# Optimization experiments

Measured on AMD Instinct MI355X. Metric: run time of the kernel, lower is better.

Reference implementation:

```python
import jax, jax.numpy as jnp
import numpy as np

N_QUBITS = 12
N_LAYERS = 2
IN_DIM = 16
BATCH = 4096
EPS = 1e-6
C64 = jnp.complex64


def _rz(t):
    return jnp.diag(jnp.stack([jnp.exp(-0.5j * t), jnp.exp(0.5j * t)]).astype(C64))


def _ry(t):
    c = jnp.cos(0.5 * t); s = jnp.sin(0.5 * t)
    return jnp.stack([jnp.stack([c, -s]), jnp.stack([s, c])]).astype(C64)


def _su2(p):
    # SU2: RZ(p0) then RY(p1) then RZ(p2)  ->  U = RZ(p2) @ RY(p1) @ RZ(p0)
    return _rz(p[2]) @ _ry(p[1]) @ _rz(p[0])


def _ising_xx(t):
    c = jnp.cos(0.5 * t).astype(C64); is_ = (-1j * jnp.sin(0.5 * t)).astype(C64)
    M = jnp.zeros((4, 4), C64)
    M = M.at[(0, 1, 2, 3), (0, 1, 2, 3)].set(c)
    M = M.at[(0, 1, 2, 3), (3, 2, 1, 0)].set(is_)
    return M


def _ising_yy(t):
    c = jnp.cos(0.5 * t).astype(C64); is_ = (-1j * jnp.sin(0.5 * t)).astype(C64)
    M = jnp.zeros((4, 4), C64)
    M = M.at[(0, 1, 2, 3), (0, 1, 2, 3)].set(c)
    M = M.at[(1, 2), (2, 1)].set(is_)
    M = M.at[(0, 3), (3, 0)].set(-is_)
    return M


def _ising_zz(t):
    sign = jnp.array([1.0, -1.0, -1.0, 1.0])
    return jnp.diag(jnp.exp(-0.5j * t * sign).astype(C64))


def _apply_1q(state, U, w):
    # state: [B] + [2]*n ; U: [2,2] (shared) or [B,2,2] (per-sample)
    st = jnp.moveaxis(state, w + 1, -1)
    if U.ndim == 2:
        st = jnp.einsum('...i,ji->...j', st, U)
    else:
        st = jnp.einsum('b...i,bji->b...j', st, U)
    return jnp.moveaxis(st, -1, w + 1)


def _apply_2q(state, U, w0, w1):
    st = jnp.moveaxis(state, (w0 + 1, w1 + 1), (-2, -1))
    shp = st.shape
    st = st.reshape(shp[:-2] + (4,))
    st = jnp.einsum('...i,ji->...j', st, U)
    return jnp.moveaxis(st.reshape(shp), (-2, -1), (w0 + 1, w1 + 1))


def _apply_zz_batched(state, theta, w0, w1):
    # IsingZZ is diagonal: multiply by per-sample phases, no matmul needed
    st = jnp.moveaxis(state, (w0 + 1, w1 + 1), (-2, -1))
    sign = jnp.array([[1.0, -1.0], [-1.0, 1.0]])
    ph = jnp.exp(-0.5j * theta[:, None, None] * sign).astype(C64)
    ph = ph.reshape((ph.shape[0],) + (1,) * (st.ndim - 3) + (2, 2))
    return jnp.moveaxis(st * ph, (-2, -1), (w0 + 1, w1 + 1))


def _forward(x, W, b, params):
    n = N_QUBITS
    B = x.shape[0]
    qfeat = x @ W.T + b  # NQE linear front-end -> [B, n_qubits] angles
    state = jnp.zeros((B, 2 ** n), C64).at[:, 0].set(1.0).reshape((B,) + (2,) * n)
    # --- data embedding (n_layers repetitions of RY + nearest-neighbor IsingZZ) ---
    c = jnp.cos(0.5 * qfeat); s = jnp.sin(0.5 * qfeat)
    for _ in range(N_LAYERS):
        for q in range(n):
            U = jnp.stack([jnp.stack([c[:, q], -s[:, q]], -1),
                           jnp.stack([s[:, q], c[:, q]], -1)], -2).astype(C64)  # [B,2,2]
            state = _apply_1q(state, U, q)
        for q in range(n - 1):
            state = _apply_zz_batched(state, qfeat[:, q] * qfeat[:, q + 1], q, q + 1)
    # --- SU4 brickwork ansatz (shared params across batch) ---
    g1 = n // 2; g2 = (n - 1) // 2
    layout = [(2 * i, 2 * i + 1) for i in range(g1)] + [(2 * i + 1, 2 * i + 2) for i in range(g2)]
    p = 0
    for a, bq in layout:
        pp = params[p:p + 15]; p += 15
        state = _apply_1q(state, _su2(pp[0:3]), a)
        state = _apply_1q(state, _su2(pp[3:6]), bq)
        state = _apply_2q(state, _ising_xx(pp[6]), a, bq)   # cartan_sign='ising'
        state = _apply_2q(state, _ising_yy(pp[7]), a, bq)
        state = _apply_2q(state, _ising_zz(pp[8]), a, bq)
        state = _apply_1q(state, _su2(pp[9:12]), a)
        state = _apply_1q(state, _su2(pp[12:15]), bq)
    state = _apply_1q(state, _su2(params[p:p + 3]), 0)
    # <Z_0> = P(q0=0) - P(q0=1)
    probs = jnp.sum(jnp.abs(state.reshape(B, 2, -1)) ** 2, axis=-1)
    y = (probs[:, 0] - probs[:, 1] + 1.0) * 0.5
    return jnp.clip(y, EPS, 1.0 - EPS)


def setup_inputs():
    key = jax.random.key(0)
    k1, k2, k3 = jax.random.split(key, 3)
    x = jax.random.normal(k1, (BATCH, IN_DIM), jnp.float32)
    W = jax.random.normal(k2, (N_QUBITS, IN_DIM), jnp.float32) * 0.3
    b = jnp.zeros((N_QUBITS,), jnp.float32)
    n_params = 15 * (N_QUBITS // 2 + (N_QUBITS - 1) // 2) + 3  # = 168
    params = jax.random.normal(k3, (n_params,), jnp.float32) * 0.1
    return {"x": x, "W": W, "b": b, "params": params}


def reference(x, W, b, params):
    return _forward(x, W, b, params)
```

## Files before the change

kernel.cpp:

```cpp
#include <hip/hip_runtime.h>
#include <math.h>

__device__ __forceinline__ float2 cmul(float2 a, float2 b) {
    return make_float2(a.x*b.x - a.y*b.y, a.x*b.y + a.y*b.x);
}
__device__ __forceinline__ float2 cadd(float2 a, float2 b) {
    return make_float2(a.x + b.x, a.y + b.y);
}
__device__ __forceinline__ float2 cfma2(float2 a, float2 b, float2 c) {
    c.x = fmaf(a.x, b.x, fmaf(-a.y, b.y, c.x));
    c.y = fmaf(a.x, b.y, fmaf( a.y, b.x, c.y));
    return c;
}

__device__ __forceinline__ void build_su2(const float* __restrict__ p, float2 U[2][2]) {
    float sb, cb;
    sincosf(0.5f * p[1], &sb, &cb);
    float ap = 0.5f * (p[0] + p[2]);
    float am = 0.5f * (p[0] - p[2]);
    float sap, cap, sam, cam;
    sincosf(ap, &sap, &cap);
    sincosf(am, &sam, &cam);
    U[0][0] = make_float2( cb * cap, -cb * sap);
    U[0][1] = make_float2(-sb * cam, -sb * sam);
    U[1][0] = make_float2( sb * cam, -sb * sam);
    U[1][1] = make_float2( cb * cap,  cb * sap);
}

__global__ void qcnn_setup(const float* __restrict__ params, float* __restrict__ g) {
    if (threadIdx.x != 0 || blockIdx.x != 0) return;
    const float* pp = params;
    float2 A1[2][2], B1[2][2], A2[2][2], B2[2][2];
    build_su2(pp + 0,  A1);
    build_su2(pp + 3,  B1);
    build_su2(pp + 9,  A2);
    build_su2(pp + 12, B2);
    float thx = pp[6], thy = pp[7], thz = pp[8];
    float Sa, Ca, Sb, Cb, sz, cz;
    sincosf(0.5f * (thx - thy), &Sa, &Ca);
    sincosf(0.5f * (thx + thy), &Sb, &Cb);
    sincosf(0.5f * thz, &sz, &cz);
    float2 pz  = make_float2(cz, -sz);
    float2 pzc = make_float2(cz,  sz);
    float2 K00 = make_float2(Ca * pz.x,  Ca * pz.y);
    float2 K03 = cmul(make_float2(0.f, -Sa), pz);
    float2 K11 = make_float2(Cb * pzc.x, Cb * pzc.y);
    float2 K12 = cmul(make_float2(0.f, -Sb), pzc);

    float2 T0[4][4], M1[4][4], T2[4][4];
    #pragma unroll
    for (int i = 0; i < 2; ++i)
        #pragma unroll
        for (int jj = 0; jj < 2; ++jj)
            #pragma unroll
            for (int k = 0; k < 2; ++k)
                #pragma unroll
                for (int l = 0; l < 2; ++l) {
                    T0[2*i+jj][2*k+l] = cmul(A1[i][k], B1[jj][l]);
                    T2[2*i+jj][2*k+l] = cmul(A2[i][k], B2[jj][l]);
                }
    #pragma unroll
    for (int c = 0; c < 4; ++c) {
        M1[0][c] = cadd(cmul(K00, T0[0][c]), cmul(K03, T0[3][c]));
        M1[1][c] = cadd(cmul(K11, T0[1][c]), cmul(K12, T0[2][c]));
        M1[2][c] = cadd(cmul(K12, T0[1][c]), cmul(K11, T0[2][c]));
        M1[3][c] = cadd(cmul(K03, T0[0][c]), cmul(K00, T0[3][c]));
    }
    #pragma unroll
    for (int r = 0; r < 4; ++r)
        #pragma unroll
        for (int c = 0; c < 4; ++c) {
            float2 a = make_float2(0.f, 0.f);
            #pragma unroll
            for (int k = 0; k < 4; ++k) a = cfma2(T2[r][k], M1[k][c], a);
            g[2*(4*r+c)]     = a.x;
            g[2*(4*r+c) + 1] = a.y;
        }

    float2 F[2][2];
    build_su2(params + 165, F);
    float n00 = F[0][0].x*F[0][0].x + F[0][0].y*F[0][0].y;
    float n10 = F[1][0].x*F[1][0].x + F[1][0].y*F[1][0].y;
    float n01 = F[0][1].x*F[0][1].x + F[0][1].y*F[0][1].y;
    float n11 = F[1][1].x*F[1][1].x + F[1][1].y*F[1][1].y;
    g[32] = n00 - n10;
    g[33] = n01 - n11;
    float mr = (F[0][0].x*F[0][1].x + F[0][0].y*F[0][1].y)
             - (F[1][0].x*F[1][1].x + F[1][0].y*F[1][1].y);
    float mi = (F[0][0].x*F[0][1].y - F[0][0].y*F[0][1].x)
             - (F[1][0].x*F[1][1].y - F[1][0].y*F[1][1].x);
    g[34] = mr;
    g[35] = mi;
}

__global__ __launch_bounds__(64) void qcnn_main(
    const float* __restrict__ x,
    const float* __restrict__ W,
    const float* __restrict__ bias,
    const float* __restrict__ g,
    float* __restrict__ out,
    int n)
{
    const int tid = blockIdx.x * 64 + threadIdx.x;
    if (tid >= n) return;

    float2 E[16];
    #pragma unroll
    for (int e = 0; e < 16; ++e) E[e] = make_float2(g[2*e], g[2*e+1]);
    const float m00 = g[32], m11 = g[33], mr = g[34], mi = g[35];

    const float* xr = x + tid * 16;
    float xv[16];
    #pragma unroll
    for (int k = 0; k < 16; ++k) xv[k] = xr[k];
    float qf[4];
    #pragma unroll
    for (int q = 0; q < 4; ++q) {
        const float* wr = W + q * 16;
        float acc = bias[q];
        #pragma unroll
        for (int k = 0; k < 16; ++k) acc = fmaf(xv[k], wr[k], acc);
        qf[q] = acc;
    }
    float c[4], s[4];
    #pragma unroll
    for (int q = 0; q < 4; ++q) sincosf(0.5f * qf[q], &s[q], &c[q]);
    float zs01, zc01, zs12, zc12, zs23, zc23;
    sincosf(0.5f * qf[0] * qf[1], &zs01, &zc01);
    sincosf(0.5f * qf[1] * qf[2], &zs12, &zc12);
    sincosf(0.5f * qf[2] * qf[3], &zs23, &zc23);
    const float2 f01e = make_float2(zc01, -zs01), f01d = make_float2(zc01, zs01);
    const float2 f12e = make_float2(zc12, -zs12), f12d = make_float2(zc12, zs12);
    const float2 f23e = make_float2(zc23, -zs23), f23d = make_float2(zc23, zs23);

    float ar[16], ai[16];
    #pragma unroll
    for (int i = 0; i < 16; ++i) {
        const int b0 = (i >> 3) & 1, b1 = (i >> 2) & 1, b2 = (i >> 1) & 1, b3 = i & 1;
        float mag = (b0 ? s[0] : c[0]) * (b1 ? s[1] : c[1])
                  * (b2 ? s[2] : c[2]) * (b3 ? s[3] : c[3]);
        float2 ph = cmul(cmul(b0 == b1 ? f01e : f01d,
                              b1 == b2 ? f12e : f12d),
                         b2 == b3 ? f23e : f23d);
        ar[i] = mag * ph.x;
        ai[i] = mag * ph.y;
    }

    #pragma unroll
    for (int p = 0; p < 16; ++p) if (!(p & 8)) {
        const int q = p | 8;
        float lr = ar[p], li = ai[p], hr = ar[q], hi = ai[q];
        ar[p] = fmaf(c[0], lr, -s[0] * hr);  ai[p] = fmaf(c[0], li, -s[0] * hi);
        ar[q] = fmaf(s[0], lr,  c[0] * hr);  ai[q] = fmaf(s[0], li,  c[0] * hi);
    }
    #pragma unroll
    for (int p = 0; p < 16; ++p) if (!(p & 4)) {
        const int q = p | 4;
        float lr = ar[p], li = ai[p], hr = ar[q], hi = ai[q];
        ar[p] = fmaf(c[1], lr, -s[1] * hr);  ai[p] = fmaf(c[1], li, -s[1] * hi);
        ar[q] = fmaf(s[1], lr,  c[1] * hr);  ai[q] = fmaf(s[1], li,  c[1] * hi);
    }
    #pragma unroll
    for (int p = 0; p < 16; ++p) if (!(p & 2)) {
        const int q = p | 2;
        float lr = ar[p], li = ai[p], hr = ar[q], hi = ai[q];
        ar[p] = fmaf(c[2], lr, -s[2] * hr);  ai[p] = fmaf(c[2], li, -s[2] * hi);
        ar[q] = fmaf(s[2], lr,  c[2] * hr);  ai[q] = fmaf(s[2], li,  c[2] * hi);
    }

    #pragma unroll
    for (int i = 0; i < 16; ++i) {
        const int b0 = (i >> 3) & 1, b1 = (i >> 2) & 1, b2 = (i >> 1) & 1;
        float2 gp = cmul(b0 == b1 ? f01e : f01d, b1 == b2 ? f12e : f12d);
        float nr = ar[i] * gp.x - ai[i] * gp.y;
        float ni = ar[i] * gp.y + ai[i] * gp.x;
        ar[i] = nr; ai[i] = ni;
    }

    #pragma unroll
    for (int gq = 0; gq < 4; ++gq) {
        float xrv[4], xiv[4];
        #pragma unroll
        for (int v = 0; v < 4; ++v) { xrv[v] = ar[(v << 2) | gq]; xiv[v] = ai[(v << 2) | gq]; }
        #pragma unroll
        for (int r = 0; r < 4; ++r) {
            float yr = 0.f, yi = 0.f;
            #pragma unroll
            for (int v = 0; v < 4; ++v) {
                const float2 m = E[r * 4 + v];
                yr = fmaf(m.x, xrv[v], fmaf(-m.y, xiv[v], yr));
                yi = fmaf(m.x, xiv[v], fmaf( m.y, xrv[v], yi));
            }
            ar[(r << 2) | gq] = yr;
            ai[(r << 2) | gq] = yi;
        }
    }

    float d = 0.f;
    #pragma unroll
    for (int i = 0; i < 8; ++i) {
        const float lr = ar[i], li = ai[i], hr = ar[i + 8], hi = ai[i + 8];
        float cross = mr * (lr * hr + li * hi) - mi * (lr * hi - li * hr);
        d += m00 * (lr * lr + li * li) + m11 * (hr * hr + hi * hi) + 2.f * cross;
    }
    float y = 0.5f * (d + 1.0f);
    out[tid] = fminf(fmaxf(y, 1e-6f), 1.0f - 1e-6f);
}

extern "C" void kernel_launch(void* const* d_in, const int* in_sizes, int n_in,
                              void* d_out, int out_size, void* d_ws, size_t ws_size,
                              hipStream_t stream) {
    (void)in_sizes; (void)n_in; (void)ws_size;
    const float* x      = (const float*)d_in[0];
    const float* W      = (const float*)d_in[1];
    const float* bias   = (const float*)d_in[2];
    const float* params = (const float*)d_in[3];
    float* out = (float*)d_out;
    float* g = (float*)d_ws;
    hipLaunchKernelGGL(qcnn_setup, dim3(1), dim3(64), 0, stream, params, g);
    hipLaunchKernelGGL(qcnn_main, dim3((out_size + 63) / 64), dim3(64), 0, stream,
                       x, W, bias, (const float*)g, out, out_size);
}
```

Baseline: 13.23 us.

## Fuse parameter setup into main kernel, computing gate matrix per block in shared memory

Drops the separate single-thread setup kernel. Each block now rebuilds the fused two-qubit gate matrix and the final measurement coefficients in parallel: 16 threads each compute one matrix entry and one thread computes the measurement terms, all written to shared memory before a barrier. Block size grows from 64 to 256 and the x row is read with float4 loads. This removes one kernel launch and the serial setup latency, at the cost of redundant per-block setup work and a __syncthreads.

```diff
diff --git a/kernel.cpp b/kernel.cpp
--- a/kernel.cpp
+++ b/kernel.cpp
@@ -1,5 +1,7 @@
 #include <hip/hip_runtime.h>
 #include <math.h>
+
+#define TPB 256
 
 __device__ __forceinline__ float2 cmul(float2 a, float2 b) {
     return make_float2(a.x*b.x - a.y*b.y, a.x*b.y + a.y*b.x);
@@ -27,99 +29,39 @@
     U[1][1] = make_float2( cb * cap,  cb * sap);
 }
 
-__global__ void qcnn_setup(const float* __restrict__ params, float* __restrict__ g) {
-    if (threadIdx.x != 0 || blockIdx.x != 0) return;
-    const float* pp = params;
-    float2 A1[2][2], B1[2][2], A2[2][2], B2[2][2];
-    build_su2(pp + 0,  A1);
-    build_su2(pp + 3,  B1);
-    build_su2(pp + 9,  A2);
-    build_su2(pp + 12, B2);
-    float thx = pp[6], thy = pp[7], thz = pp[8];
-    float Sa, Ca, Sb, Cb, sz, cz;
-    sincosf(0.5f * (thx - thy), &Sa, &Ca);
-    sincosf(0.5f * (thx + thy), &Sb, &Cb);
-    sincosf(0.5f * thz, &sz, &cz);
-    float2 pz  = make_float2(cz, -sz);
-    float2 pzc = make_float2(cz,  sz);
-    float2 K00 = make_float2(Ca * pz.x,  Ca * pz.y);
-    float2 K03 = cmul(make_float2(0.f, -Sa), pz);
-    float2 K11 = make_float2(Cb * pzc.x, Cb * pzc.y);
-    float2 K12 = cmul(make_float2(0.f, -Sb), pzc);
-
-    float2 T0[4][4], M1[4][4], T2[4][4];
-    #pragma unroll
-    for (int i = 0; i < 2; ++i)
-        #pragma unroll
-        for (int jj = 0; jj < 2; ++jj)
-            #pragma unroll
-            for (int k = 0; k < 2; ++k)
-                #pragma unroll
-                for (int l = 0; l < 2; ++l) {
-                    T0[2*i+jj][2*k+l] = cmul(A1[i][k], B1[jj][l]);
-                    T2[2*i+jj][2*k+l] = cmul(A2[i][k], B2[jj][l]);
-                }
-    #pragma unroll
-    for (int c = 0; c < 4; ++c) {
-        M1[0][c] = cadd(cmul(K00, T0[0][c]), cmul(K03, T0[3][c]));
-        M1[1][c] = cadd(cmul(K11, T0[1][c]), cmul(K12, T0[2][c]));
-        M1[2][c] = cadd(cmul(K12, T0[1][c]), cmul(K11, T0[2][c]));
-        M1[3][c] = cadd(cmul(K03, T0[0][c]), cmul(K00, T0[3][c]));
-    }
-    #pragma unroll
-    for (int r = 0; r < 4; ++r)
-        #pragma unroll
-        for (int c = 0; c < 4; ++c) {
-            float2 a = make_float2(0.f, 0.f);
-            #pragma unroll
-            for (int k = 0; k < 4; ++k) a = cfma2(T2[r][k], M1[k][c], a);
-            g[2*(4*r+c)]     = a.x;
-            g[2*(4*r+c) + 1] = a.y;
-        }
-
-    float2 F[2][2];
-    build_su2(params + 165, F);
-    float n00 = F[0][0].x*F[0][0].x + F[0][0].y*F[0][0].y;
-    float n10 = F[1][0].x*F[1][0].x + F[1][0].y*F[1][0].y;
-    float n01 = F[0][1].x*F[0][1].x + F[0][1].y*F[0][1].y;
-    float n11 = F[1][1].x*F[1][1].x + F[1][1].y*F[1][1].y;
-    g[32] = n00 - n10;
-    g[33] = n01 - n11;
-    float mr = (F[0][0].x*F[0][1].x + F[0][0].y*F[0][1].y)
-             - (F[1][0].x*F[1][1].x + F[1][0].y*F[1][1].y);
-    float mi = (F[0][0].x*F[0][1].y - F[0][0].y*F[0][1].x)
-             - (F[1][0].x*F[1][1].y - F[1][0].y*F[1][1].x);
-    g[34] = mr;
-    g[35] = mi;
-}
-
-__global__ __launch_bounds__(64) void qcnn_main(
+__global__ __launch_bounds__(TPB) void qcnn_fused(
     const float* __restrict__ x,
     const float* __restrict__ W,
     const float* __restrict__ bias,
-    const float* __restrict__ g,
+    const float* __restrict__ params,
     float* __restrict__ out,
     int n)
 {
-    const int tid = blockIdx.x * 64 + threadIdx.x;
-    if (tid >= n) return;
-
-    float2 E[16];
-    #pragma unroll
-    for (int e = 0; e < 16; ++e) E[e] = make_float2(g[2*e], g[2*e+1]);
-    const float m00 = g[32], m11 = g[33], mr = g[34], mi = g[35];
-
-    const float* xr = x + tid * 16;
-    float xv[16];
-    #pragma unroll
-    for (int k = 0; k < 16; ++k) xv[k] = xr[k];
+    __shared__ float2 sE[16];
+    __shared__ float  sM[4];
+
+    const int t   = threadIdx.x;
+    const int tid = blockIdx.x * TPB + t;
+    const int row = (tid < n) ? tid : (n - 1);
+
+    const float* xr = x + row * 16;
+    const float4 xv0 = *(const float4*)(xr + 0);
+    const float4 xv1 = *(const float4*)(xr + 4);
+    const float4 xv2 = *(const float4*)(xr + 8);
+    const float4 xv3 = *(const float4*)(xr + 12);
     float qf[4];
     #pragma unroll
     for (int q = 0; q < 4; ++q) {
         const float* wr = W + q * 16;
         float acc = bias[q];
-        #pragma unroll
-        for (int k = 0; k < 16; ++k) acc = fmaf(xv[k], wr[k], acc);
+        acc = fmaf(xv0.x, wr[0],  acc); acc = fmaf(xv0.y, wr[1],  acc);
+        acc = fmaf(xv0.z, wr[2],  acc); acc = fmaf(xv0.w, wr[3],  acc);
+        acc = fmaf(xv1.x, wr[4],  acc); acc = fmaf(xv1.y, wr[5],  acc);
+        acc = fmaf(xv1.z, wr[6],  acc); acc = fmaf(xv1.w, wr[7],  acc);
+        acc = fmaf(xv2.x, wr[8],  acc); acc = fmaf(xv2.y, wr[9],  acc);
+        acc = fmaf(xv2.z, wr[10], acc); acc = fmaf(xv2.w, wr[11], acc);
+        acc = fmaf(xv3.x, wr[12], acc); acc = fmaf(xv3.y, wr[13], acc);
+        acc = fmaf(xv3.z, wr[14], acc); acc = fmaf(xv3.w, wr[15], acc);
         qf[q] = acc;
     }
     float c[4], s[4];
@@ -132,6 +74,61 @@
     const float2 f01e = make_float2(zc01, -zs01), f01d = make_float2(zc01, zs01);
     const float2 f12e = make_float2(zc12, -zs12), f12d = make_float2(zc12, zs12);
     const float2 f23e = make_float2(zc23, -zs23), f23d = make_float2(zc23, zs23);
+
+    if (t < 16) {
+        const float* pp = params;
+        float2 A1[2][2], B1[2][2], A2[2][2], B2[2][2];
+        build_su2(pp + 0,  A1);
+        build_su2(pp + 3,  B1);
+        build_su2(pp + 9,  A2);
+        build_su2(pp + 12, B2);
+        const float thx = pp[6], thy = pp[7], thz = pp[8];
+        float Sa, Ca, Sb, Cb, sz, cz;
+        sincosf(0.5f * (thx - thy), &Sa, &Ca);
+        sincosf(0.5f * (thx + thy), &Sb, &Cb);
+        sincosf(0.5f * thz, &sz, &cz);
+        const float2 pz  = make_float2(cz, -sz);
+        const float2 pzc = make_float2(cz,  sz);
+        const float2 K00 = make_float2(Ca * pz.x,  Ca * pz.y);
+        const float2 K03 = cmul(make_float2(0.f, -Sa), pz);
+        const float2 K11 = make_float2(Cb * pzc.x, Cb * pzc.y);
+        const float2 K12 = cmul(make_float2(0.f, -Sb), pzc);
+
+        const int r = t >> 2, cc = t & 3;
+        float2 T0c[4];
+        #pragma unroll
+        for (int j = 0; j < 4; ++j)
+            T0c[j] = cmul(A1[j >> 1][cc >> 1], B1[j & 1][cc & 1]);
+        float2 M1c[4];
+        M1c[0] = cadd(cmul(K00, T0c[0]), cmul(K03, T0c[3]));
+        M1c[1] = cadd(cmul(K11, T0c[1]), cmul(K12, T0c[2]));
+        M1c[2] = cadd(cmul(K12, T0c[1]), cmul(K11, T0c[2]));
+        M1c[3] = cadd(cmul(K03, T0c[0]), cmul(K00, T0c[3]));
+        float2 acc = make_float2(0.f, 0.f);
+        #pragma unroll
+        for (int k = 0; k < 4; ++k)
+            acc = cfma2(cmul(A2[r >> 1][k >> 1], B2[r & 1][k & 1]), M1c[k], acc);
+        sE[t] = acc;
+    } else if (t == 16) {
+        float2 F[2][2];
+        build_su2(params + 165, F);
+        const float n00 = F[0][0].x*F[0][0].x + F[0][0].y*F[0][0].y;
+        const float n10 = F[1][0].x*F[1][0].x + F[1][0].y*F[1][0].y;
+        const float n01 = F[0][1].x*F[0][1].x + F[0][1].y*F[0][1].y;
+        const float n11 = F[1][1].x*F[1][1].x + F[1][1].y*F[1][1].y;
+        sM[0] = n00 - n10;
+        sM[1] = n01 - n11;
+        sM[2] = (F[0][0].x*F[0][1].x + F[0][0].y*F[0][1].y)
+              - (F[1][0].x*F[1][1].x + F[1][0].y*F[1][1].y);
+        sM[3] = (F[0][0].x*F[0][1].y - F[0][0].y*F[0][1].x)
+              - (F[1][0].x*F[1][1].y - F[1][0].y*F[1][1].x);
+    }
+    __syncthreads();
+
+    float2 E[16];
+    #pragma unroll
+    for (int e = 0; e < 16; ++e) E[e] = sE[e];
+    const float m00 = sM[0], m11 = sM[1], mr = sM[2], mi = sM[3];
 
     float ar[16], ai[16];
     #pragma unroll
@@ -204,20 +201,19 @@
         d += m00 * (lr * lr + li * li) + m11 * (hr * hr + hi * hi) + 2.f * cross;
     }
     float y = 0.5f * (d + 1.0f);
-    out[tid] = fminf(fmaxf(y, 1e-6f), 1.0f - 1e-6f);
+    y = fminf(fmaxf(y, 1e-6f), 1.0f - 1e-6f);
+    if (tid < n) out[tid] = y;
 }
 
 extern "C" void kernel_launch(void* const* d_in, const int* in_sizes, int n_in,
                               void* d_out, int out_size, void* d_ws, size_t ws_size,
                               hipStream_t stream) {
-    (void)in_sizes; (void)n_in; (void)ws_size;
+    (void)in_sizes; (void)n_in; (void)d_ws; (void)ws_size;
     const float* x      = (const float*)d_in[0];
     const float* W      = (const float*)d_in[1];
     const float* bias   = (const float*)d_in[2];
     const float* params = (const float*)d_in[3];
     float* out = (float*)d_out;
-    float* g = (float*)d_ws;
-    hipLaunchKernelGGL(qcnn_setup, dim3(1), dim3(64), 0, stream, params, g);
-    hipLaunchKernelGGL(qcnn_main, dim3((out_size + 63) / 64), dim3(64), 0, stream,
-                       x, W, bias, (const float*)g, out, out_size);
-}
+    hipLaunchKernelGGL(qcnn_fused, dim3((out_size + TPB - 1) / TPB), dim3(TPB), 0, stream,
+                       x, W, bias, params, out, out_size);
+}
```

New measurement: 14.66 us. 10.8% more time.
